# Kernel optimization log

Hardware: AMD Instinct MI355X
Metric: run time of the kernel (lower is better)

Reference implementation:

```python
import jax, jax.numpy as jnp
import numpy as np

N, E, D, G = 50000, 600000, 128, 64
EPS = 1e-5


def prelu(x, a):
    return jnp.where(x >= 0, x, a * x)


def degree_norms(edge_src, edge_dst):
    ones = jnp.ones((E,), jnp.float32)
    deg_out = jax.ops.segment_sum(ones, edge_src, num_segments=N)
    deg_in = jax.ops.segment_sum(ones, edge_dst, num_segments=N)
    norm_src = jnp.where(deg_out > 0, jax.lax.rsqrt(jnp.maximum(deg_out, 1.0)), 0.0)
    norm_dst = jnp.where(deg_in > 0, jax.lax.rsqrt(jnp.maximum(deg_in, 1.0)), 0.0)
    return norm_src, norm_dst


def graph_conv(x, W, b, alpha, edge_src, edge_dst, norm_src, norm_dst):
    # DGL GraphConv norm='both': D_out^{-1/2} on src, aggregate, D_in^{-1/2} on dst, then linear
    xs = x * norm_src[:, None]
    agg = jax.ops.segment_sum(xs[edge_src], edge_dst, num_segments=N)
    agg = agg * norm_dst[:, None]
    h = agg @ W + b
    return prelu(h, alpha)


def batch_norm(h, gamma, beta):
    mean = jnp.mean(h, axis=0)
    var = jnp.mean(jnp.square(h - mean), axis=0)
    return (h - mean) * jax.lax.rsqrt(var + EPS) * gamma + beta


def setup_inputs() -> dict:
    key = jax.random.key(0)
    ks = jax.random.split(key, 8)
    inp = {
        "heat": jax.random.normal(ks[0], (N, D), jnp.float32),
        "edge_src": jax.random.randint(ks[1], (E,), 0, N, jnp.int32),
        "edge_dst": jax.random.randint(ks[2], (E,), 0, N, jnp.int32),
        "graph_ids": jnp.sort(jax.random.randint(ks[3], (N,), 0, G, jnp.int32)),
    }
    for i in range(2):
        kw = jax.random.fold_in(ks[4], i)
        inp[f"W{i}"] = jax.random.normal(kw, (D, D), jnp.float32) * (1.0 / np.sqrt(D))
        inp[f"b{i}"] = jnp.zeros((D,), jnp.float32)
        inp[f"ac{i}"] = jnp.float32(0.25)  # conv PReLU alpha
        inp[f"g{i}"] = jnp.ones((D,), jnp.float32)
        inp[f"be{i}"] = jnp.zeros((D,), jnp.float32)
        inp[f"aa{i}"] = jnp.float32(0.25)  # outer PReLU alpha
    return inp


def reference(heat, edge_src, edge_dst, graph_ids,
              W0, b0, ac0, g0, be0, aa0,
              W1, b1, ac1, g1, be1, aa1):
    norm_src, norm_dst = degree_norms(edge_src, edge_dst)
    x = heat  # dropout in eval mode -> identity
    h = graph_conv(x, W0, b0, ac0, edge_src, edge_dst, norm_src, norm_dst)
    h = prelu(batch_norm(h, g0, be0), aa0)
    gh = jax.ops.segment_sum(h, graph_ids, num_segments=G)
    h = graph_conv(h, W1, b1, ac1, edge_src, edge_dst, norm_src, norm_dst)
    h = prelu(batch_norm(h, g1, be1), aa1)
    gh = gh + jax.ops.segment_sum(h, graph_ids, num_segments=G)
    return h, gh
```

## Files before the change

kernel.cpp:

```cpp
#include <hip/hip_runtime.h>

#define NN 50000
#define NE 600000
#define DD 128
#define GG 64
#define EPS 1e-5f
#define CAP 64
#define HB 64
#define HALF 25000
#define HWORDS 12500

typedef unsigned short u16;
typedef unsigned int u32;
typedef u16 u16x8 __attribute__((ext_vector_type(8)));
typedef short bf16x8 __attribute__((ext_vector_type(8)));
typedef float f32x4 __attribute__((ext_vector_type(4)));

__device__ __forceinline__ float bf2f(u16 v) {
    return __uint_as_float(((u32)v) << 16);
}
__device__ __forceinline__ u16 f2bf(float f) {
    u32 u = __float_as_uint(f);
    u += 0x7fff + ((u >> 16) & 1);
    return (u16)(u >> 16);
}

__global__ void k_wprep(const float* __restrict__ W0, const float* __restrict__ W1,
                        u16* __restrict__ wtb, int* __restrict__ cnt_in,
                        float* __restrict__ stats , float* __restrict__ gh) {
    int k = threadIdx.x;
    int c = blockIdx.x;
    int lay = blockIdx.y;
    const float* W = lay ? W1 : W0;
    wtb[lay * DD * DD + c * DD + k] = f2bf(W[k * DD + c]);

    int gtid = (blockIdx.y * gridDim.x + blockIdx.x) * DD + threadIdx.x;
    for (int i = gtid; i < NN; i += 32768) cnt_in[i] = 0;
    if (gtid < 4 * DD) stats[gtid] = 0.f;
    if (gtid < GG * DD) gh[gtid] = 0.f;
}

__global__ __launch_bounds__(256) void k_hist(const int* __restrict__ src,
                                              u32* __restrict__ partials) {
    __shared__ u32 hc[HWORDS];
    int t = threadIdx.x, b = blockIdx.x, p = blockIdx.y;
    for (int i = t; i < HWORDS; i += 256) hc[i] = 0;
    __syncthreads();
    int lo = p * HALF;
    int e0 = b * (NE / HB);
    for (int e = e0 + t; e < e0 + NE / HB; e += 256) {
        int s = src[e] - lo;
        if ((u32)s < (u32)HALF) atomicAdd(&hc[s >> 1], 1u << ((s & 1) << 4));
    }
    __syncthreads();
    u32* out = partials + (size_t)(p * HB + b) * HWORDS;
    for (int i = t; i < HWORDS; i += 256) out[i] = hc[i];
}

__global__ void k_hist_reduce(const u32* __restrict__ partials, const int* __restrict__ cnt_in,
                              float* __restrict__ norm_src, float* __restrict__ norm_dst) {
    int j = blockIdx.x * 256 + threadIdx.x;
    int p = blockIdx.y;
    if (j < HWORDS) {
        u32 s = 0;
#pragma unroll 8
        for (int b = 0; b < HB; ++b) s += partials[(size_t)(p * HB + b) * HWORDS + j];
        int n0 = p * HALF + 2 * j;
        u32 c0 = s & 0xffffu, c1 = s >> 16;
        norm_src[n0]     = c0 ? rsqrtf((float)c0) : 0.f;
        norm_src[n0 + 1] = c1 ? rsqrtf((float)c1) : 0.f;
        int d0 = cnt_in[n0], d1 = cnt_in[n0 + 1];
        norm_dst[n0]     = d0 > 0 ? rsqrtf((float)d0) : 0.f;
        norm_dst[n0 + 1] = d1 > 0 ? rsqrtf((float)d1) : 0.f;
    }
}

__global__ void k_build(const int* __restrict__ src, const int* __restrict__ dst,
                        int* __restrict__ cnt_in, u16* __restrict__ csr) {
    int e = blockIdx.x * 256 + threadIdx.x;
    if (e < NE) {
        int d = dst[e];
        int pos = atomicAdd(&cnt_in[d], 1);
        if (pos < CAP) csr[(size_t)d * CAP + pos] = (u16)src[e];
    }
}

__global__ void k_scale_rows(const float* __restrict__ norm_src, const float* __restrict__ x,
                             u16* __restrict__ xsb) {
    int idx = blockIdx.x * 256 + threadIdx.x;
    int row = idx >> 4;
    int c8 = (idx & 15) << 3;
    float ns = norm_src[row];
    const float4* xp = (const float4*)(x + (size_t)row * DD + c8);
    float4 a = xp[0], b = xp[1];
    u16x8 o;
    o[0] = f2bf(a.x * ns); o[1] = f2bf(a.y * ns); o[2] = f2bf(a.z * ns); o[3] = f2bf(a.w * ns);
    o[4] = f2bf(b.x * ns); o[5] = f2bf(b.y * ns); o[6] = f2bf(b.z * ns); o[7] = f2bf(b.w * ns);
    *(u16x8*)(xsb + (size_t)idx * 8) = o;
}

__global__ __launch_bounds__(256) void k_gg(
        const u16* __restrict__ xsb, const int* __restrict__ cnt_in,
        const u16* __restrict__ csr, const float* __restrict__ norm_dst,
        const u16* __restrict__ wtb, const float* __restrict__ bias,
        const float* __restrict__ ac, u16* __restrict__ hpreb,
        float* __restrict__ sums, float* __restrict__ sumsq) {
    __shared__ u16 sAg[4][16][DD + 8];
    __shared__ float sStat[2][4][DD];
    int t = threadIdx.x;
    int w = t >> 6;
    int l = t & 63;
    int rb = blockIdx.x * 64 + w * 16;
    bool wvalid = (rb < NN);
    int cl = l & 15;
    int rr = l >> 4;
    const u16* xcol = xsb + cl * 8;

    if (wvalid) {
#pragma unroll
        for (int g = 0; g < 4; ++g) {
            int r = rb + g * 4 + rr;
            int cnt = min(cnt_in[r], CAP);
            const u16* ce = csr + (size_t)r * CAP;
            float acc[8] = {0.f, 0.f, 0.f, 0.f, 0.f, 0.f, 0.f, 0.f};
            int e = 0;
            for (; e + 8 <= cnt; e += 8) {
                u16x8 ii = *(const u16x8*)(ce + e);
                u16x8 v0 = *(const u16x8*)(xcol + (size_t)ii[0] * DD);
                u16x8 v1 = *(const u16x8*)(xcol + (size_t)ii[1] * DD);
                u16x8 v2 = *(const u16x8*)(xcol + (size_t)ii[2] * DD);
                u16x8 v3 = *(const u16x8*)(xcol + (size_t)ii[3] * DD);
                u16x8 v4 = *(const u16x8*)(xcol + (size_t)ii[4] * DD);
                u16x8 v5 = *(const u16x8*)(xcol + (size_t)ii[5] * DD);
                u16x8 v6 = *(const u16x8*)(xcol + (size_t)ii[6] * DD);
                u16x8 v7 = *(const u16x8*)(xcol + (size_t)ii[7] * DD);
#pragma unroll
                for (int j = 0; j < 8; ++j) {
                    float a01 = bf2f(v0[j]) + bf2f(v1[j]);
                    float a23 = bf2f(v2[j]) + bf2f(v3[j]);
                    float a45 = bf2f(v4[j]) + bf2f(v5[j]);
                    float a67 = bf2f(v6[j]) + bf2f(v7[j]);
                    acc[j] += (a01 + a23) + (a45 + a67);
                }
            }
            for (; e + 2 <= cnt; e += 2) {
                int s0 = ce[e], s1 = ce[e + 1];
                u16x8 v0 = *(const u16x8*)(xcol + (size_t)s0 * DD);
                u16x8 v1 = *(const u16x8*)(xcol + (size_t)s1 * DD);
#pragma unroll
                for (int j = 0; j < 8; ++j) acc[j] += bf2f(v0[j]) + bf2f(v1[j]);
            }
            if (e < cnt) {
                int s0 = ce[e];
                u16x8 v0 = *(const u16x8*)(xcol + (size_t)s0 * DD);
#pragma unroll
                for (int j = 0; j < 8; ++j) acc[j] += bf2f(v0[j]);
            }
            float nd = norm_dst[r];
            u16x8 o;
#pragma unroll
            for (int j = 0; j < 8; ++j) o[j] = f2bf(acc[j] * nd);
            *(u16x8*)&sAg[w][g * 4 + rr][cl * 8] = o;
        }
    }
    __syncthreads();

    int lr = cl;
    int kg = rr;
    float alpha = ac[0];

    bf16x8 afrag[4];
    if (wvalid) {
        const u16* abase = &sAg[w][lr][kg * 8];
        afrag[0] = *(const bf16x8*)(abase);
        afrag[1] = *(const bf16x8*)(abase + 32);
        afrag[2] = *(const bf16x8*)(abase + 64);
        afrag[3] = *(const bf16x8*)(abase + 96);
    }

#pragma unroll
    for (int ct = 0; ct < 8; ++ct) {
        int c = ct * 16;
        float sS = 0.f, sQ = 0.f;
        if (wvalid) {
            const u16* bbase = wtb + (size_t)(c + lr) * DD + kg * 8;
            bf16x8 b0 = *(const bf16x8*)(bbase);
            bf16x8 b1 = *(const bf16x8*)(bbase + 32);
            bf16x8 b2 = *(const bf16x8*)(bbase + 64);
            bf16x8 b3 = *(const bf16x8*)(bbase + 96);
            float bv = bias[c + lr];
            f32x4 acc = {bv, bv, bv, bv};
            acc = __builtin_amdgcn_mfma_f32_16x16x32_bf16(afrag[0], b0, acc, 0, 0, 0);
            acc = __builtin_amdgcn_mfma_f32_16x16x32_bf16(afrag[1], b1, acc, 0, 0, 0);
            acc = __builtin_amdgcn_mfma_f32_16x16x32_bf16(afrag[2], b2, acc, 0, 0, 0);
            acc = __builtin_amdgcn_mfma_f32_16x16x32_bf16(afrag[3], b3, acc, 0, 0, 0);
#pragma unroll
            for (int j = 0; j < 4; ++j) {
                float h = acc[j];
                h = h >= 0.f ? h : alpha * h;
                u16 hb = f2bf(h);
                float hq = bf2f(hb);
                int grow = rb + kg * 4 + j;
                hpreb[(size_t)grow * DD + c + lr] = hb;
                sS += hq;
                sQ += hq * hq;
            }
        }
        sS += __shfl_xor(sS, 16); sS += __shfl_xor(sS, 32);
        sQ += __shfl_xor(sQ, 16); sQ += __shfl_xor(sQ, 32);
        if (kg == 0) {
            sStat[0][w][c + lr] = sS;
            sStat[1][w][c + lr] = sQ;
        }
    }
    __syncthreads();
    if (t < DD) {
        float s = sStat[0][0][t] + sStat[0][1][t] + sStat[0][2][t] + sStat[0][3][t];
        atomicAdd(&sums[t], s);
    } else if (t < 2 * DD) {
        int c = t - DD;
        float q = sStat[1][0][c] + sStat[1][1][c] + sStat[1][2][c] + sStat[1][3][c];
        atomicAdd(&sumsq[c], q);
    }
}

__global__ void k_bn_prelu(const u16* __restrict__ hpreb,
                           const float* __restrict__ sums, const float* __restrict__ sumsq,
                           const float* __restrict__ gamma, const float* __restrict__ beta,
                           const float* __restrict__ aa, const float* __restrict__ nsrc,
                           float* __restrict__ h_out, u16* __restrict__ xs_next, int writeXs) {
    __shared__ float sc[DD], sh[DD];
    int t = threadIdx.x;
    if (t < DD) {
        float mean = sums[t] * (1.0f / NN);
        float var = sumsq[t] * (1.0f / NN) - mean * mean;
        float inv = rsqrtf(var + EPS);
        float s = inv * gamma[t];
        sc[t] = s;
        sh[t] = beta[t] - mean * s;
    }
    __syncthreads();
    int idx = blockIdx.x * 256 + t;
    int row = idx >> 4;
    int c8 = (idx & 15) << 3;
    float a = aa[0];
    u16x8 hv = *(const u16x8*)(hpreb + (size_t)idx * 8);
    float v[8];
#pragma unroll
    for (int j = 0; j < 8; ++j) v[j] = bf2f(hv[j]) * sc[c8 + j] + sh[c8 + j];
#pragma unroll
    for (int j = 0; j < 8; ++j) v[j] = v[j] >= 0.f ? v[j] : a * v[j];
    float4* op = (float4*)(h_out + (size_t)idx * 8);
    op[0] = make_float4(v[0], v[1], v[2], v[3]);
    op[1] = make_float4(v[4], v[5], v[6], v[7]);
    if (writeXs) {
        float ns = nsrc[row];
        u16x8 o;
#pragma unroll
        for (int j = 0; j < 8; ++j) o[j] = f2bf(v[j] * ns);
        *(u16x8*)(xs_next + (size_t)idx * 8) = o;
    }
}

__global__ void k_seg(const u16* __restrict__ hpreb, const int* __restrict__ gids,
                      const float* __restrict__ sums, const float* __restrict__ sumsq,
                      const float* __restrict__ gamma, const float* __restrict__ beta,
                      const float* __restrict__ aa, float* __restrict__ gh) {
    __shared__ float red[2][DD];
    __shared__ float sc[DD], sh[DD];
    int t = threadIdx.x;
    if (t < DD) {
        float mean = sums[t] * (1.0f / NN);
        float var = sumsq[t] * (1.0f / NN) - mean * mean;
        float inv = rsqrtf(var + EPS);
        float s = inv * gamma[t];
        sc[t] = s;
        sh[t] = beta[t] - mean * s;
    }
    __syncthreads();
    int g = blockIdx.x;
    int slice = blockIdx.y;
    int lo, hi;
    {
        int l = 0, r = NN;
        while (l < r) { int m = (l + r) >> 1; if (gids[m] < g) l = m + 1; else r = m; }
        lo = l;
        r = NN;
        while (l < r) { int m = (l + r) >> 1; if (gids[m] < g + 1) l = m + 1; else r = m; }
        hi = l;
    }
    int cnt = hi - lo;
    int chunk = (cnt + 7) >> 3;
    int s0 = lo + slice * chunk;
    int s1 = min(s0 + chunk, hi);
    float a = aa[0];
    int c = t & 127;
    int half = t >> 7;
    float s = 0.f;
    for (int row = s0 + half; row < s1; row += 2) {
        float v = bf2f(hpreb[(size_t)row * DD + c]) * sc[c] + sh[c];
        v = v >= 0.f ? v : a * v;
        s += v;
    }
    red[half][c] = s;
    __syncthreads();
    if (t < DD)
        atomicAdd(&gh[g * DD + t], red[0][t] + red[1][t]);
}

extern "C" void kernel_launch(void* const* d_in, const int* in_sizes, int n_in,
                              void* d_out, int out_size, void* d_ws, size_t ws_size,
                              hipStream_t stream) {
    const float* heat = (const float*)d_in[0];
    const int* esrc = (const int*)d_in[1];
    const int* edst = (const int*)d_in[2];
    const int* gids = (const int*)d_in[3];
    const float* Wp[2]  = {(const float*)d_in[4],  (const float*)d_in[10]};
    const float* bp[2]  = {(const float*)d_in[5],  (const float*)d_in[11]};
    const float* acp[2] = {(const float*)d_in[6],  (const float*)d_in[12]};
    const float* gp[2]  = {(const float*)d_in[7],  (const float*)d_in[13]};
    const float* bep[2] = {(const float*)d_in[8],  (const float*)d_in[14]};
    const float* aap[2] = {(const float*)d_in[9],  (const float*)d_in[15]};

    float* out = (float*)d_out;
    float* h_out = out;
    float* gh = out + (size_t)NN * DD;

    char* wsp = (char*)d_ws;
    int* cnt_in_i   = (int*)wsp;              wsp += NN * sizeof(int);
    float* norm_src = (float*)wsp;            wsp += NN * sizeof(float);
    float* norm_dst = (float*)wsp;            wsp += NN * sizeof(float);
    float* stats    = (float*)wsp;            wsp += 4 * DD * sizeof(float);
    u16* wtb        = (u16*)wsp;              wsp += 2 * DD * DD * sizeof(u16);
    u16* xsb        = (u16*)wsp;              wsp += (size_t)NN * DD * sizeof(u16);
    u16* hpreb      = (u16*)wsp;              wsp += (size_t)NN * DD * sizeof(u16);
    u16* csr        = (u16*)wsp;              wsp += (size_t)NN * CAP * sizeof(u16);
    u32* partials   = (u32*)wsp;              wsp += (size_t)2 * HB * HWORDS * sizeof(u32);

    dim3 gwp(DD, 2);
    k_wprep<<<gwp, DD, 0, stream>>>(Wp[0], Wp[1], wtb, cnt_in_i, stats, gh);
    dim3 ghist(HB, 2);
    k_hist<<<ghist, 256, 0, stream>>>(esrc, partials);
    k_build<<<(NE + 255) / 256, 256, 0, stream>>>(esrc, edst, cnt_in_i, csr);
    dim3 gred((HWORDS + 255) / 256, 2);
    k_hist_reduce<<<gred, 256, 0, stream>>>(partials, cnt_in_i, norm_src, norm_dst);
    k_scale_rows<<<NN * 16 / 256, 256, 0, stream>>>(norm_src, heat, xsb);

    for (int layer = 0; layer < 2; ++layer) {
        float* sums_l  = stats + layer * 2 * DD;
        float* sumsq_l = sums_l + DD;
        k_gg<<<(NN + 63) / 64, 256, 0, stream>>>(xsb, cnt_in_i, csr, norm_dst,
                                                 wtb + layer * DD * DD, bp[layer], acp[layer],
                                                 hpreb, sums_l, sumsq_l);
        k_bn_prelu<<<NN * 16 / 256, 256, 0, stream>>>(hpreb, sums_l, sumsq_l,
                                                      gp[layer], bep[layer], aap[layer],
                                                      norm_src, h_out, xsb, layer == 0 ? 1 : 0);
        dim3 gseg(GG, 8);
        k_seg<<<gseg, 256, 0, stream>>>(hpreb, gids, sums_l, sumsq_l,
                                        gp[layer], bep[layer], aap[layer], gh);
    }
}
```

Baseline: 244.0 us.

## Pad CSR with zero-row sentinel and halve rows per gather-GEMM block

Pre-fills the CSR neighbour lists with a sentinel index pointing to an appended all-zero row of the scaled feature buffer, so the gather loop always processes groups of 8 and drops the scalar tail loops. The fused gather+GEMM kernel now handles 32 rows per block, with pairs of waves sharing a 16-row tile and each wave doing half of the output columns. This doubles the block count for better occupancy and latency hiding, and removes tail branching. The cost is extra zero-row loads for padded slots and an additional CSR fill pass in the prep kernel.

```diff
diff --git a/kernel.cpp b/kernel.cpp
--- a/kernel.cpp
+++ b/kernel.cpp
@@ -9,6 +9,8 @@
 #define HB 64
 #define HALF 25000
 #define HWORDS 12500
+#define ZROW 50000
+#define ZFILL 0xC350C350u
 
 typedef unsigned short u16;
 typedef unsigned int u32;
@@ -27,7 +29,8 @@
 
 __global__ void k_wprep(const float* __restrict__ W0, const float* __restrict__ W1,
                         u16* __restrict__ wtb, int* __restrict__ cnt_in,
-                        float* __restrict__ stats , float* __restrict__ gh) {
+                        float* __restrict__ stats , float* __restrict__ gh,
+                        u32* __restrict__ csr32, u16* __restrict__ xsb) {
     int k = threadIdx.x;
     int c = blockIdx.x;
     int lay = blockIdx.y;
@@ -36,8 +39,13 @@
 
     int gtid = (blockIdx.y * gridDim.x + blockIdx.x) * DD + threadIdx.x;
     for (int i = gtid; i < NN; i += 32768) cnt_in[i] = 0;
+    for (int i = gtid; i < NN * CAP / 2; i += 32768) csr32[i] = ZFILL;
     if (gtid < 4 * DD) stats[gtid] = 0.f;
     if (gtid < GG * DD) gh[gtid] = 0.f;
+    if (gtid < DD / 8) {
+        u16x8 z = {0, 0, 0, 0, 0, 0, 0, 0};
+        *(u16x8*)(xsb + (size_t)ZROW * DD + gtid * 8) = z;
+    }
 }
 
 __global__ __launch_bounds__(256) void k_hist(const int* __restrict__ src,
@@ -105,12 +113,14 @@
         const u16* __restrict__ wtb, const float* __restrict__ bias,
         const float* __restrict__ ac, u16* __restrict__ hpreb,
         float* __restrict__ sums, float* __restrict__ sumsq) {
-    __shared__ u16 sAg[4][16][DD + 8];
+    __shared__ u16 sAg[2][16][DD + 8];
     __shared__ float sStat[2][4][DD];
     int t = threadIdx.x;
     int w = t >> 6;
     int l = t & 63;
-    int rb = blockIdx.x * 64 + w * 16;
+    int g2 = w >> 1;
+    int ch = w & 1;
+    int rb = blockIdx.x * 32 + g2 * 16;
     bool wvalid = (rb < NN);
     int cl = l & 15;
     int rr = l >> 4;
@@ -118,13 +128,13 @@
 
     if (wvalid) {
 #pragma unroll
-        for (int g = 0; g < 4; ++g) {
-            int r = rb + g * 4 + rr;
+        for (int g = 0; g < 2; ++g) {
+            int rloc = ch * 8 + g * 4 + rr;
+            int r = rb + rloc;
             int cnt = min(cnt_in[r], CAP);
             const u16* ce = csr + (size_t)r * CAP;
             float acc[8] = {0.f, 0.f, 0.f, 0.f, 0.f, 0.f, 0.f, 0.f};
-            int e = 0;
-            for (; e + 8 <= cnt; e += 8) {
+            for (int e = 0; e < cnt; e += 8) {
                 u16x8 ii = *(const u16x8*)(ce + e);
                 u16x8 v0 = *(const u16x8*)(xcol + (size_t)ii[0] * DD);
                 u16x8 v1 = *(const u16x8*)(xcol + (size_t)ii[1] * DD);
@@ -143,24 +153,11 @@
                     acc[j] += (a01 + a23) + (a45 + a67);
                 }
             }
-            for (; e + 2 <= cnt; e += 2) {
-                int s0 = ce[e], s1 = ce[e + 1];
-                u16x8 v0 = *(const u16x8*)(xcol + (size_t)s0 * DD);
-                u16x8 v1 = *(const u16x8*)(xcol + (size_t)s1 * DD);
-#pragma unroll
-                for (int j = 0; j < 8; ++j) acc[j] += bf2f(v0[j]) + bf2f(v1[j]);
-            }
-            if (e < cnt) {
-                int s0 = ce[e];
-                u16x8 v0 = *(const u16x8*)(xcol + (size_t)s0 * DD);
-#pragma unroll
-                for (int j = 0; j < 8; ++j) acc[j] += bf2f(v0[j]);
-            }
             float nd = norm_dst[r];
             u16x8 o;
 #pragma unroll
             for (int j = 0; j < 8; ++j) o[j] = f2bf(acc[j] * nd);
-            *(u16x8*)&sAg[w][g * 4 + rr][cl * 8] = o;
+            *(u16x8*)&sAg[g2][rloc][cl * 8] = o;
         }
     }
     __syncthreads();
@@ -171,7 +168,7 @@
 
     bf16x8 afrag[4];
     if (wvalid) {
-        const u16* abase = &sAg[w][lr][kg * 8];
+        const u16* abase = &sAg[g2][lr][kg * 8];
         afrag[0] = *(const bf16x8*)(abase);
         afrag[1] = *(const bf16x8*)(abase + 32);
         afrag[2] = *(const bf16x8*)(abase + 64);
@@ -179,8 +176,8 @@
     }
 
 #pragma unroll
-    for (int ct = 0; ct < 8; ++ct) {
-        int c = ct * 16;
+    for (int ct = 0; ct < 4; ++ct) {
+        int c = ch * 64 + ct * 16;
         float sS = 0.f, sQ = 0.f;
         if (wvalid) {
             const u16* bbase = wtb + (size_t)(c + lr) * DD + kg * 8;
@@ -215,12 +212,12 @@
     }
     __syncthreads();
     if (t < DD) {
-        float s = sStat[0][0][t] + sStat[0][1][t] + sStat[0][2][t] + sStat[0][3][t];
-        atomicAdd(&sums[t], s);
+        int hi = t >> 6;
+        atomicAdd(&sums[t], sStat[0][hi][t] + sStat[0][2 + hi][t]);
     } else if (t < 2 * DD) {
         int c = t - DD;
-        float q = sStat[1][0][c] + sStat[1][1][c] + sStat[1][2][c] + sStat[1][3][c];
-        atomicAdd(&sumsq[c], q);
+        int hi = c >> 6;
+        atomicAdd(&sumsq[c], sStat[1][hi][c] + sStat[1][2 + hi][c]);
     }
 }
 
@@ -332,13 +329,14 @@
     float* norm_dst = (float*)wsp;            wsp += NN * sizeof(float);
     float* stats    = (float*)wsp;            wsp += 4 * DD * sizeof(float);
     u16* wtb        = (u16*)wsp;              wsp += 2 * DD * DD * sizeof(u16);
-    u16* xsb        = (u16*)wsp;              wsp += (size_t)NN * DD * sizeof(u16);
+    u16* xsb        = (u16*)wsp;              wsp += (size_t)(NN + 1) * DD * sizeof(u16);
     u16* hpreb      = (u16*)wsp;              wsp += (size_t)NN * DD * sizeof(u16);
     u16* csr        = (u16*)wsp;              wsp += (size_t)NN * CAP * sizeof(u16);
     u32* partials   = (u32*)wsp;              wsp += (size_t)2 * HB * HWORDS * sizeof(u32);
 
     dim3 gwp(DD, 2);
-    k_wprep<<<gwp, DD, 0, stream>>>(Wp[0], Wp[1], wtb, cnt_in_i, stats, gh);
+    k_wprep<<<gwp, DD, 0, stream>>>(Wp[0], Wp[1], wtb, cnt_in_i, stats, gh,
+                                    (u32*)csr, xsb);
     dim3 ghist(HB, 2);
     k_hist<<<ghist, 256, 0, stream>>>(esrc, partials);
     k_build<<<(NE + 255) / 256, 256, 0, stream>>>(esrc, edst, cnt_in_i, csr);
@@ -349,7 +347,7 @@
     for (int layer = 0; layer < 2; ++layer) {
         float* sums_l  = stats + layer * 2 * DD;
         float* sumsq_l = sums_l + DD;
-        k_gg<<<(NN + 63) / 64, 256, 0, stream>>>(xsb, cnt_in_i, csr, norm_dst,
+        k_gg<<<(NN + 31) / 32, 256, 0, stream>>>(xsb, cnt_in_i, csr, norm_dst,
                                                  wtb + layer * DD * DD, bp[layer], acp[layer],
                                                  hpreb, sums_l, sumsq_l);
         k_bn_prelu<<<NN * 16 / 256, 256, 0, stream>>>(hpreb, sums_l, sumsq_l,
```

Measured after the change: 270.0 us. 1.11x slower.
